# Kernel tuning notes

Measured on AMD Instinct MI355X. Metric: run time of the kernel, lower is better.

## Reference

```python
import jax, jax.numpy as jnp
import numpy as np

B, H, N, F_IN, F_OUT, M = 32, 24, 500, 64, 4, 16
O = H * N  # n_instances


def setup_inputs() -> dict:
    key = jax.random.key(0)
    ks = jax.random.split(key, 6)
    s = 1.0 / np.sqrt(F_IN)
    return {
        "x": jax.random.normal(ks[0], (B, H, N, F_IN), dtype=jnp.float32),
        "mu_w": jax.random.normal(ks[1], (O, F_IN, F_OUT), dtype=jnp.float32) * s,
        "mu_b": jax.random.normal(ks[2], (O, F_OUT), dtype=jnp.float32) * s,
        "sigma_w": jax.random.normal(ks[3], (O, F_IN, F_OUT * F_OUT), dtype=jnp.float32) * s,
        "sigma_b": jax.random.normal(ks[4], (O, F_OUT * F_OUT), dtype=jnp.float32) * s,
        "eps": jax.random.normal(ks[5], (M, B, H, N, F_OUT), dtype=jnp.float32),
    }


def reference(x, mu_w, mu_b, sigma_w, sigma_b, eps):
    b = x.shape[0]
    x_ = x.reshape(b, O, F_IN)  # '... h n f -> ... (h n) f'
    # per-instance linear: mu[b,o,:] = x[b,o,:] @ mu_w[o] + mu_b[o]
    mu = jnp.einsum('bof,ofg->bog', x_, mu_w) + mu_b  # [b, o, F_OUT]
    mu = mu.reshape(b, H, N, F_OUT)
    sigma = jnp.einsum('bof,ofk->bok', x_, sigma_w) + sigma_b  # [b, o, F_OUT^2]
    sigma = sigma.reshape(b, H, N, F_OUT, F_OUT)  # [..., l, f]
    # out[m,b,h,n,l] = mu + sum_f sigma[b,h,n,l,f] * eps[m,b,h,n,f]
    out = mu[None] + jnp.einsum('bhnlf,mbhnf->mbhnl', sigma, eps)
    return out
```

## Files before the change

### kernel.cpp

```cpp
#include <hip/hip_runtime.h>

#define Bc   32
#define Oc   12000
#define Mc   16

__global__ __launch_bounds__(256) void mgr_fused_kernel(
    const float* __restrict__ x,
    const float* __restrict__ mu_w,
    const float* __restrict__ mu_b,
    const float* __restrict__ sigma_w,
    const float* __restrict__ sigma_b,
    const float* __restrict__ eps,
    float* __restrict__ out)
{
    __shared__ float4 s_sw4[8 * 257];
    __shared__ float4 s_muw4[8 * 65];
    __shared__ float4 s_mub4[8];
    __shared__ float4 s_sb4[8 * 4];

    const int tid = threadIdx.x;
    const int blk = blockIdx.x;

    const float4* __restrict__ g_sw4 = reinterpret_cast<const float4*>(sigma_w) + blk * 2048;
    #pragma unroll
    for (int it = 0; it < 8; ++it)
        s_sw4[it * 257 + tid] = g_sw4[it * 256 + tid];

    const float4* __restrict__ g_muw4 = reinterpret_cast<const float4*>(mu_w) + blk * 512;
    #pragma unroll
    for (int it = 0; it < 2; ++it) {
        int g = it * 256 + tid;
        s_muw4[(g >> 6) * 65 + (g & 63)] = g_muw4[g];
    }

    if (tid < 32) {
        s_sb4[tid] = reinterpret_cast<const float4*>(sigma_b)[blk * 32 + tid];
    } else if (tid < 40) {
        s_mub4[tid - 32] = reinterpret_cast<const float4*>(mu_b)[blk * 8 + (tid - 32)];
    }

    const int oi = tid & 7;
    const int bi = tid >> 3;
    const int o  = blk * 8 + oi;

    const float4* __restrict__ x4 = reinterpret_cast<const float4*>(x) + (bi * Oc + o) * 16;
    float4 xv[16];
    #pragma unroll
    for (int i = 0; i < 16; ++i) xv[i] = x4[i];

    __syncthreads();

    float4 amu = s_mub4[oi];
    float4 as0 = s_sb4[oi * 4 + 0];
    float4 as1 = s_sb4[oi * 4 + 1];
    float4 as2 = s_sb4[oi * 4 + 2];
    float4 as3 = s_sb4[oi * 4 + 3];

    const float4* __restrict__ muw = &s_muw4[oi * 65];
    const float4* __restrict__ sw  = &s_sw4[oi * 257];

    #pragma unroll
    for (int fo = 0; fo < 16; ++fo) {
        const float4 xq = xv[fo];
        #pragma unroll
        for (int fi = 0; fi < 4; ++fi) {
            const int f = 4 * fo + fi;
            const float xs = (fi == 0) ? xq.x : (fi == 1) ? xq.y : (fi == 2) ? xq.z : xq.w;
            float4 w = muw[f];
            amu.x = fmaf(xs, w.x, amu.x);
            amu.y = fmaf(xs, w.y, amu.y);
            amu.z = fmaf(xs, w.z, amu.z);
            amu.w = fmaf(xs, w.w, amu.w);
            float4 s;
            s = sw[4 * f + 0];
            as0.x = fmaf(xs, s.x, as0.x); as0.y = fmaf(xs, s.y, as0.y);
            as0.z = fmaf(xs, s.z, as0.z); as0.w = fmaf(xs, s.w, as0.w);
            s = sw[4 * f + 1];
            as1.x = fmaf(xs, s.x, as1.x); as1.y = fmaf(xs, s.y, as1.y);
            as1.z = fmaf(xs, s.z, as1.z); as1.w = fmaf(xs, s.w, as1.w);
            s = sw[4 * f + 2];
            as2.x = fmaf(xs, s.x, as2.x); as2.y = fmaf(xs, s.y, as2.y);
            as2.z = fmaf(xs, s.z, as2.z); as2.w = fmaf(xs, s.w, as2.w);
            s = sw[4 * f + 3];
            as3.x = fmaf(xs, s.x, as3.x); as3.y = fmaf(xs, s.y, as3.y);
            as3.z = fmaf(xs, s.z, as3.z); as3.w = fmaf(xs, s.w, as3.w);
        }
    }

    const float4* __restrict__ eps4 = reinterpret_cast<const float4*>(eps);
    float4* __restrict__ out4 = reinterpret_cast<float4*>(out);

    #pragma unroll 4
    for (int m = 0; m < Mc; ++m) {
        const int idx = (m * Bc + bi) * Oc + o;
        float4 e = eps4[idx];
        float4 r;
        r.x = amu.x + as0.x * e.x + as0.y * e.y + as0.z * e.z + as0.w * e.w;
        r.y = amu.y + as1.x * e.x + as1.y * e.y + as1.z * e.z + as1.w * e.w;
        r.z = amu.z + as2.x * e.x + as2.y * e.y + as2.z * e.z + as2.w * e.w;
        r.w = amu.w + as3.x * e.x + as3.y * e.y + as3.z * e.z + as3.w * e.w;
        out4[idx] = r;
    }
}

extern "C" void kernel_launch(void* const* d_in, const int* in_sizes, int n_in,
                              void* d_out, int out_size, void* d_ws, size_t ws_size,
                              hipStream_t stream) {
    const float* x       = (const float*)d_in[0];
    const float* mu_w    = (const float*)d_in[1];
    const float* mu_b    = (const float*)d_in[2];
    const float* sigma_w = (const float*)d_in[3];
    const float* sigma_b = (const float*)d_in[4];
    const float* eps     = (const float*)d_in[5];
    float* out = (float*)d_out;

    dim3 grid(Oc / 8);
    dim3 block(256);
    mgr_fused_kernel<<<grid, block, 0, stream>>>(x, mu_w, mu_b, sigma_w, sigma_b, eps, out);
}
```

Measured before the change: 291.9 us.

## Drop shared-memory weight staging; each thread handles two batches per instance

Weights are no longer staged in LDS. Each thread reads its instance's mu_w and sigma_w straight from global memory and reuses each weight value for two batch rows, with 16 instances per block instead of 8. This removes the LDS fill, the barrier and the LDS capacity limit on occupancy, and launch bounds now request 3 blocks per CU. In exchange, each thread's weight reads are strided per instance rather than coalesced, so it relies on L1/L2 for reuse across the 16 threads sharing an instance, and it uses more accumulator registers.

```diff
diff --git a/kernel.cpp b/kernel.cpp
--- a/kernel.cpp
+++ b/kernel.cpp
@@ -4,7 +4,7 @@
 #define Oc   12000
 #define Mc   16
 
-__global__ __launch_bounds__(256) void mgr_fused_kernel(
+__global__ __launch_bounds__(256, 3) void mgr_fused_kernel(
     const float* __restrict__ x,
     const float* __restrict__ mu_w,
     const float* __restrict__ mu_b,
@@ -13,77 +13,62 @@
     const float* __restrict__ eps,
     float* __restrict__ out)
 {
-    __shared__ float4 s_sw4[8 * 257];
-    __shared__ float4 s_muw4[8 * 65];
-    __shared__ float4 s_mub4[8];
-    __shared__ float4 s_sb4[8 * 4];
+    const int tid = threadIdx.x;
+    const int oi  = tid & 15;
+    const int bg  = tid >> 4;
+    const int o   = blockIdx.x * 16 + oi;
+    const int b0  = bg;
+    const int b1  = bg + 16;
 
-    const int tid = threadIdx.x;
-    const int blk = blockIdx.x;
+    const float4* __restrict__ muw4 = reinterpret_cast<const float4*>(mu_w) + o * 64;
+    const float4* __restrict__ sw4  = reinterpret_cast<const float4*>(sigma_w) + o * 256;
+    const float4* __restrict__ x40  = reinterpret_cast<const float4*>(x) + (b0 * Oc + o) * 16;
+    const float4* __restrict__ x41  = reinterpret_cast<const float4*>(x) + (b1 * Oc + o) * 16;
 
-    const float4* __restrict__ g_sw4 = reinterpret_cast<const float4*>(sigma_w) + blk * 2048;
-    #pragma unroll
-    for (int it = 0; it < 8; ++it)
-        s_sw4[it * 257 + tid] = g_sw4[it * 256 + tid];
+    float4 amu0 = reinterpret_cast<const float4*>(mu_b)[o];
+    float4 amu1 = amu0;
+    float4 a00 = reinterpret_cast<const float4*>(sigma_b)[o * 4 + 0]; float4 a10 = a00;
+    float4 a01 = reinterpret_cast<const float4*>(sigma_b)[o * 4 + 1]; float4 a11 = a01;
+    float4 a02 = reinterpret_cast<const float4*>(sigma_b)[o * 4 + 2]; float4 a12 = a02;
+    float4 a03 = reinterpret_cast<const float4*>(sigma_b)[o * 4 + 3]; float4 a13 = a03;
 
-    const float4* __restrict__ g_muw4 = reinterpret_cast<const float4*>(mu_w) + blk * 512;
-    #pragma unroll
-    for (int it = 0; it < 2; ++it) {
-        int g = it * 256 + tid;
-        s_muw4[(g >> 6) * 65 + (g & 63)] = g_muw4[g];
-    }
-
-    if (tid < 32) {
-        s_sb4[tid] = reinterpret_cast<const float4*>(sigma_b)[blk * 32 + tid];
-    } else if (tid < 40) {
-        s_mub4[tid - 32] = reinterpret_cast<const float4*>(mu_b)[blk * 8 + (tid - 32)];
-    }
-
-    const int oi = tid & 7;
-    const int bi = tid >> 3;
-    const int o  = blk * 8 + oi;
-
-    const float4* __restrict__ x4 = reinterpret_cast<const float4*>(x) + (bi * Oc + o) * 16;
-    float4 xv[16];
-    #pragma unroll
-    for (int i = 0; i < 16; ++i) xv[i] = x4[i];
-
-    __syncthreads();
-
-    float4 amu = s_mub4[oi];
-    float4 as0 = s_sb4[oi * 4 + 0];
-    float4 as1 = s_sb4[oi * 4 + 1];
-    float4 as2 = s_sb4[oi * 4 + 2];
-    float4 as3 = s_sb4[oi * 4 + 3];
-
-    const float4* __restrict__ muw = &s_muw4[oi * 65];
-    const float4* __restrict__ sw  = &s_sw4[oi * 257];
-
-    #pragma unroll
+    #pragma unroll 4
     for (int fo = 0; fo < 16; ++fo) {
-        const float4 xq = xv[fo];
+        const float4 xq0 = x40[fo];
+        const float4 xq1 = x41[fo];
         #pragma unroll
         for (int fi = 0; fi < 4; ++fi) {
             const int f = 4 * fo + fi;
-            const float xs = (fi == 0) ? xq.x : (fi == 1) ? xq.y : (fi == 2) ? xq.z : xq.w;
-            float4 w = muw[f];
-            amu.x = fmaf(xs, w.x, amu.x);
-            amu.y = fmaf(xs, w.y, amu.y);
-            amu.z = fmaf(xs, w.z, amu.z);
-            amu.w = fmaf(xs, w.w, amu.w);
+            const float xs0 = (fi == 0) ? xq0.x : (fi == 1) ? xq0.y : (fi == 2) ? xq0.z : xq0.w;
+            const float xs1 = (fi == 0) ? xq1.x : (fi == 1) ? xq1.y : (fi == 2) ? xq1.z : xq1.w;
+
+            float4 w = muw4[f];
+            amu0.x = fmaf(xs0, w.x, amu0.x); amu0.y = fmaf(xs0, w.y, amu0.y);
+            amu0.z = fmaf(xs0, w.z, amu0.z); amu0.w = fmaf(xs0, w.w, amu0.w);
+            amu1.x = fmaf(xs1, w.x, amu1.x); amu1.y = fmaf(xs1, w.y, amu1.y);
+            amu1.z = fmaf(xs1, w.z, amu1.z); amu1.w = fmaf(xs1, w.w, amu1.w);
+
             float4 s;
-            s = sw[4 * f + 0];
-            as0.x = fmaf(xs, s.x, as0.x); as0.y = fmaf(xs, s.y, as0.y);
-            as0.z = fmaf(xs, s.z, as0.z); as0.w = fmaf(xs, s.w, as0.w);
-            s = sw[4 * f + 1];
-            as1.x = fmaf(xs, s.x, as1.x); as1.y = fmaf(xs, s.y, as1.y);
-            as1.z = fmaf(xs, s.z, as1.z); as1.w = fmaf(xs, s.w, as1.w);
-            s = sw[4 * f + 2];
-            as2.x = fmaf(xs, s.x, as2.x); as2.y = fmaf(xs, s.y, as2.y);
-            as2.z = fmaf(xs, s.z, as2.z); as2.w = fmaf(xs, s.w, as2.w);
-            s = sw[4 * f + 3];
-            as3.x = fmaf(xs, s.x, as3.x); as3.y = fmaf(xs, s.y, as3.y);
-            as3.z = fmaf(xs, s.z, as3.z); as3.w = fmaf(xs, s.w, as3.w);
+            s = sw4[4 * f + 0];
+            a00.x = fmaf(xs0, s.x, a00.x); a00.y = fmaf(xs0, s.y, a00.y);
+            a00.z = fmaf(xs0, s.z, a00.z); a00.w = fmaf(xs0, s.w, a00.w);
+            a10.x = fmaf(xs1, s.x, a10.x); a10.y = fmaf(xs1, s.y, a10.y);
+            a10.z = fmaf(xs1, s.z, a10.z); a10.w = fmaf(xs1, s.w, a10.w);
+            s = sw4[4 * f + 1];
+            a01.x = fmaf(xs0, s.x, a01.x); a01.y = fmaf(xs0, s.y, a01.y);
+            a01.z = fmaf(xs0, s.z, a01.z); a01.w = fmaf(xs0, s.w, a01.w);
+            a11.x = fmaf(xs1, s.x, a11.x); a11.y = fmaf(xs1, s.y, a11.y);
+            a11.z = fmaf(xs1, s.z, a11.z); a11.w = fmaf(xs1, s.w, a11.w);
+            s = sw4[4 * f + 2];
+            a02.x = fmaf(xs0, s.x, a02.x); a02.y = fmaf(xs0, s.y, a02.y);
+            a02.z = fmaf(xs0, s.z, a02.z); a02.w = fmaf(xs0, s.w, a02.w);
+            a12.x = fmaf(xs1, s.x, a12.x); a12.y = fmaf(xs1, s.y, a12.y);
+            a12.z = fmaf(xs1, s.z, a12.z); a12.w = fmaf(xs1, s.w, a12.w);
+            s = sw4[4 * f + 3];
+            a03.x = fmaf(xs0, s.x, a03.x); a03.y = fmaf(xs0, s.y, a03.y);
+            a03.z = fmaf(xs0, s.z, a03.z); a03.w = fmaf(xs0, s.w, a03.w);
+            a13.x = fmaf(xs1, s.x, a13.x); a13.y = fmaf(xs1, s.y, a13.y);
+            a13.z = fmaf(xs1, s.z, a13.z); a13.w = fmaf(xs1, s.w, a13.w);
         }
     }
 
@@ -92,14 +77,21 @@
 
     #pragma unroll 4
     for (int m = 0; m < Mc; ++m) {
-        const int idx = (m * Bc + bi) * Oc + o;
-        float4 e = eps4[idx];
-        float4 r;
-        r.x = amu.x + as0.x * e.x + as0.y * e.y + as0.z * e.z + as0.w * e.w;
-        r.y = amu.y + as1.x * e.x + as1.y * e.y + as1.z * e.z + as1.w * e.w;
-        r.z = amu.z + as2.x * e.x + as2.y * e.y + as2.z * e.z + as2.w * e.w;
-        r.w = amu.w + as3.x * e.x + as3.y * e.y + as3.z * e.z + as3.w * e.w;
-        out4[idx] = r;
+        const int i0 = (m * Bc + b0) * Oc + o;
+        const int i1 = (m * Bc + b1) * Oc + o;
+        const float4 e0 = eps4[i0];
+        const float4 e1 = eps4[i1];
+        float4 r0, r1;
+        r0.x = amu0.x + a00.x * e0.x + a00.y * e0.y + a00.z * e0.z + a00.w * e0.w;
+        r0.y = amu0.y + a01.x * e0.x + a01.y * e0.y + a01.z * e0.z + a01.w * e0.w;
+        r0.z = amu0.z + a02.x * e0.x + a02.y * e0.y + a02.z * e0.z + a02.w * e0.w;
+        r0.w = amu0.w + a03.x * e0.x + a03.y * e0.y + a03.z * e0.z + a03.w * e0.w;
+        r1.x = amu1.x + a10.x * e1.x + a10.y * e1.y + a10.z * e1.z + a10.w * e1.w;
+        r1.y = amu1.y + a11.x * e1.x + a11.y * e1.y + a11.z * e1.z + a11.w * e1.w;
+        r1.z = amu1.z + a12.x * e1.x + a12.y * e1.y + a12.z * e1.z + a12.w * e1.w;
+        r1.w = amu1.w + a13.x * e1.x + a13.y * e1.y + a13.z * e1.z + a13.w * e1.w;
+        out4[i0] = r0;
+        out4[i1] = r1;
     }
 }
 
@@ -114,7 +106,7 @@
     const float* eps     = (const float*)d_in[5];
     float* out = (float*)d_out;
 
-    dim3 grid(Oc / 8);
+    dim3 grid(Oc / 16);
     dim3 block(256);
     mgr_fused_kernel<<<grid, block, 0, stream>>>(x, mu_w, mu_b, sigma_w, sigma_b, eps, out);
 }
```

Result: slower. 358.1 us (+22.7%).

## Chunk weight staging over F_IN to shrink LDS and raise occupancy

Applied to the files above, without the earlier changes.

Stages sigma_w and mu_w into shared memory in four 16-feature chunks instead of all at once, cutting LDS per block roughly fourfold. It loads x in chunks rather than holding all 16 float4 in registers, and sets launch_bounds min-blocks to 4 so more blocks stay resident and hide memory latency. All 16 eps float4 loads are issued up front before computing outputs, to raise memory-level parallelism. The cost is extra __syncthreads per chunk and more registers for the eps prefetch, which could force spills under the new launch bound.

```diff
diff --git a/kernel.cpp b/kernel.cpp
--- a/kernel.cpp
+++ b/kernel.cpp
@@ -4,7 +4,7 @@
 #define Oc   12000
 #define Mc   16
 
-__global__ __launch_bounds__(256) void mgr_fused_kernel(
+__global__ __launch_bounds__(256, 4) void mgr_fused_kernel(
     const float* __restrict__ x,
     const float* __restrict__ mu_w,
     const float* __restrict__ mu_b,
@@ -13,92 +13,108 @@
     const float* __restrict__ eps,
     float* __restrict__ out)
 {
-    __shared__ float4 s_sw4[8 * 257];
-    __shared__ float4 s_muw4[8 * 65];
+    __shared__ float4 s_sw4[8 * 65];
+    __shared__ float4 s_muw4[8 * 17];
     __shared__ float4 s_mub4[8];
     __shared__ float4 s_sb4[8 * 4];
 
     const int tid = threadIdx.x;
     const int blk = blockIdx.x;
+    const int oi  = tid & 7;
+    const int bi  = tid >> 3;
+    const int o   = blk * 8 + oi;
 
-    const float4* __restrict__ g_sw4 = reinterpret_cast<const float4*>(sigma_w) + blk * 2048;
-    #pragma unroll
-    for (int it = 0; it < 8; ++it)
-        s_sw4[it * 257 + tid] = g_sw4[it * 256 + tid];
+    const float4* __restrict__ sw_g  = reinterpret_cast<const float4*>(sigma_w) + blk * 8 * 256;
+    const float4* __restrict__ muw_g = reinterpret_cast<const float4*>(mu_w)    + blk * 8 * 64;
+    const float4* __restrict__ x4    = reinterpret_cast<const float4*>(x) + (bi * Oc + o) * 16;
 
-    const float4* __restrict__ g_muw4 = reinterpret_cast<const float4*>(mu_w) + blk * 512;
-    #pragma unroll
-    for (int it = 0; it < 2; ++it) {
-        int g = it * 256 + tid;
-        s_muw4[(g >> 6) * 65 + (g & 63)] = g_muw4[g];
-    }
-
-    if (tid < 32) {
-        s_sb4[tid] = reinterpret_cast<const float4*>(sigma_b)[blk * 32 + tid];
-    } else if (tid < 40) {
-        s_mub4[tid - 32] = reinterpret_cast<const float4*>(mu_b)[blk * 8 + (tid - 32)];
-    }
-
-    const int oi = tid & 7;
-    const int bi = tid >> 3;
-    const int o  = blk * 8 + oi;
-
-    const float4* __restrict__ x4 = reinterpret_cast<const float4*>(x) + (bi * Oc + o) * 16;
-    float4 xv[16];
-    #pragma unroll
-    for (int i = 0; i < 16; ++i) xv[i] = x4[i];
-
-    __syncthreads();
-
-    float4 amu = s_mub4[oi];
-    float4 as0 = s_sb4[oi * 4 + 0];
-    float4 as1 = s_sb4[oi * 4 + 1];
-    float4 as2 = s_sb4[oi * 4 + 2];
-    float4 as3 = s_sb4[oi * 4 + 3];
-
-    const float4* __restrict__ muw = &s_muw4[oi * 65];
-    const float4* __restrict__ sw  = &s_sw4[oi * 257];
+    float4 amu, as0, as1, as2, as3;
 
     #pragma unroll
-    for (int fo = 0; fo < 16; ++fo) {
-        const float4 xq = xv[fo];
+    for (int c = 0; c < 4; ++c) {
+        if (c > 0) __syncthreads();
+
+        const float4 xv0 = x4[c * 4 + 0];
+        const float4 xv1 = x4[c * 4 + 1];
+        const float4 xv2 = x4[c * 4 + 2];
+        const float4 xv3 = x4[c * 4 + 3];
+
+        {
+            const int t0 = tid, t1 = tid + 256;
+            const float4 v0 = sw_g[(t0 >> 6) * 256 + c * 64 + (t0 & 63)];
+            const float4 v1 = sw_g[(t1 >> 6) * 256 + c * 64 + (t1 & 63)];
+            s_sw4[(t0 >> 6) * 65 + (t0 & 63)] = v0;
+            s_sw4[(t1 >> 6) * 65 + (t1 & 63)] = v1;
+        }
+        if (tid < 128) {
+            const int oL = tid >> 4, fl = tid & 15;
+            s_muw4[oL * 17 + fl] = muw_g[oL * 64 + c * 16 + fl];
+        }
+        if (c == 0) {
+            if (tid < 32) {
+                s_sb4[tid] = reinterpret_cast<const float4*>(sigma_b)[blk * 32 + tid];
+            } else if (tid < 40) {
+                s_mub4[tid - 32] = reinterpret_cast<const float4*>(mu_b)[blk * 8 + (tid - 32)];
+            }
+        }
+        __syncthreads();
+
+        if (c == 0) {
+            amu = s_mub4[oi];
+            as0 = s_sb4[oi * 4 + 0];
+            as1 = s_sb4[oi * 4 + 1];
+            as2 = s_sb4[oi * 4 + 2];
+            as3 = s_sb4[oi * 4 + 3];
+        }
+
+        const float4* __restrict__ muw = &s_muw4[oi * 17];
+        const float4* __restrict__ sw  = &s_sw4[oi * 65];
+
         #pragma unroll
-        for (int fi = 0; fi < 4; ++fi) {
-            const int f = 4 * fo + fi;
-            const float xs = (fi == 0) ? xq.x : (fi == 1) ? xq.y : (fi == 2) ? xq.z : xq.w;
-            float4 w = muw[f];
-            amu.x = fmaf(xs, w.x, amu.x);
-            amu.y = fmaf(xs, w.y, amu.y);
-            amu.z = fmaf(xs, w.z, amu.z);
-            amu.w = fmaf(xs, w.w, amu.w);
-            float4 s;
-            s = sw[4 * f + 0];
-            as0.x = fmaf(xs, s.x, as0.x); as0.y = fmaf(xs, s.y, as0.y);
-            as0.z = fmaf(xs, s.z, as0.z); as0.w = fmaf(xs, s.w, as0.w);
-            s = sw[4 * f + 1];
-            as1.x = fmaf(xs, s.x, as1.x); as1.y = fmaf(xs, s.y, as1.y);
-            as1.z = fmaf(xs, s.z, as1.z); as1.w = fmaf(xs, s.w, as1.w);
-            s = sw[4 * f + 2];
-            as2.x = fmaf(xs, s.x, as2.x); as2.y = fmaf(xs, s.y, as2.y);
-            as2.z = fmaf(xs, s.z, as2.z); as2.w = fmaf(xs, s.w, as2.w);
-            s = sw[4 * f + 3];
-            as3.x = fmaf(xs, s.x, as3.x); as3.y = fmaf(xs, s.y, as3.y);
-            as3.z = fmaf(xs, s.z, as3.z); as3.w = fmaf(xs, s.w, as3.w);
+        for (int fq = 0; fq < 4; ++fq) {
+            const float4 xq = (fq == 0) ? xv0 : (fq == 1) ? xv1 : (fq == 2) ? xv2 : xv3;
+            #pragma unroll
+            for (int fi = 0; fi < 4; ++fi) {
+                const int fl = fq * 4 + fi;
+                const float xs = (fi == 0) ? xq.x : (fi == 1) ? xq.y : (fi == 2) ? xq.z : xq.w;
+                float4 w = muw[fl];
+                amu.x = fmaf(xs, w.x, amu.x);
+                amu.y = fmaf(xs, w.y, amu.y);
+                amu.z = fmaf(xs, w.z, amu.z);
+                amu.w = fmaf(xs, w.w, amu.w);
+                float4 s;
+                s = sw[4 * fl + 0];
+                as0.x = fmaf(xs, s.x, as0.x); as0.y = fmaf(xs, s.y, as0.y);
+                as0.z = fmaf(xs, s.z, as0.z); as0.w = fmaf(xs, s.w, as0.w);
+                s = sw[4 * fl + 1];
+                as1.x = fmaf(xs, s.x, as1.x); as1.y = fmaf(xs, s.y, as1.y);
+                as1.z = fmaf(xs, s.z, as1.z); as1.w = fmaf(xs, s.w, as1.w);
+                s = sw[4 * fl + 2];
+                as2.x = fmaf(xs, s.x, as2.x); as2.y = fmaf(xs, s.y, as2.y);
+                as2.z = fmaf(xs, s.z, as2.z); as2.w = fmaf(xs, s.w, as2.w);
+                s = sw[4 * fl + 3];
+                as3.x = fmaf(xs, s.x, as3.x); as3.y = fmaf(xs, s.y, as3.y);
+                as3.z = fmaf(xs, s.z, as3.z); as3.w = fmaf(xs, s.w, as3.w);
+            }
         }
     }
 
     const float4* __restrict__ eps4 = reinterpret_cast<const float4*>(eps);
     float4* __restrict__ out4 = reinterpret_cast<float4*>(out);
 
-    #pragma unroll 4
+    float4 e[16];
+    #pragma unroll
+    for (int m = 0; m < Mc; ++m)
+        e[m] = eps4[(m * Bc + bi) * Oc + o];
+
+    #pragma unroll
     for (int m = 0; m < Mc; ++m) {
         const int idx = (m * Bc + bi) * Oc + o;
-        float4 e = eps4[idx];
         float4 r;
-        r.x = amu.x + as0.x * e.x + as0.y * e.y + as0.z * e.z + as0.w * e.w;
-        r.y = amu.y + as1.x * e.x + as1.y * e.y + as1.z * e.z + as1.w * e.w;
-        r.z = amu.z + as2.x * e.x + as2.y * e.y + as2.z * e.z + as2.w * e.w;
-        r.w = amu.w + as3.x * e.x + as3.y * e.y + as3.z * e.z + as3.w * e.w;
+        r.x = amu.x + as0.x * e[m].x + as0.y * e[m].y + as0.z * e[m].z + as0.w * e[m].w;
+        r.y = amu.y + as1.x * e[m].x + as1.y * e[m].y + as1.z * e[m].z + as1.w * e[m].w;
+        r.z = amu.z + as2.x * e[m].x + as2.y * e[m].y + as2.z * e[m].z + as2.w * e[m].w;
+        r.w = amu.w + as3.x * e[m].x + as3.y * e[m].y + as3.z * e[m].z + as3.w * e[m].w;
         out4[idx] = r;
     }
 }
```

Measured after the change: 899.5 us. +208.1%, slower.
